# Optimization experiments

Measured on AMD Instinct MI355X. Metric: run time of the kernel, lower is better.

The kernel has to match this reference:

```python
import jax, jax.numpy as jnp
import numpy as np

N_NODES = 50000
N_EDGES = 800000
D_FEAT = 128


def setup_inputs() -> dict:
    key = jax.random.key(0)
    k1, k2, k3, k4, k5, k6 = jax.random.split(key, 6)
    input = jax.random.normal(k1, (N_NODES, D_FEAT), dtype=jnp.float32)
    h0 = jax.random.normal(k2, (N_NODES, D_FEAT), dtype=jnp.float32)
    # edge list + weights represent the sparse normalized adjacency used by torch.spmm
    edge_row = jax.random.randint(k3, (N_EDGES,), 0, N_NODES, dtype=jnp.int32)
    edge_col = jax.random.randint(k4, (N_EDGES,), 0, N_NODES, dtype=jnp.int32)
    edge_weight = jax.random.uniform(k5, (N_EDGES,), dtype=jnp.float32)
    # learned parameter: uniform(-stdv, stdv) with stdv = 1/sqrt(out_features)
    stdv = 1.0 / np.sqrt(D_FEAT)
    weight = jax.random.uniform(k6, (D_FEAT, D_FEAT), dtype=jnp.float32,
                                minval=-stdv, maxval=stdv)
    return {
        "input": input,
        "h0": h0,
        "weight": weight,
        "edge_row": edge_row,
        "edge_col": edge_col,
        "edge_weight": edge_weight,
        "lamda": jnp.float32(0.5),
        "alpha": jnp.float32(0.1),
        "l": 4,
    }


def reference(input, h0, weight, edge_row, edge_col, edge_weight, lamda, alpha, l):
    n = input.shape[0]
    # theta = min(1, log(lamda / l + 1))
    theta = jnp.minimum(jnp.float32(1.0), jnp.log(lamda / l + 1.0))
    # hi = spmm(adj, input): gather source features, scale by edge weight, scatter-add to dest rows
    hi = jax.ops.segment_sum(edge_weight[:, None] * input[edge_col], edge_row,
                             num_segments=n)  # [N, D]
    support = (1.0 - alpha) * hi + alpha * h0
    output = theta * (support @ weight) + (1.0 - theta) * support
    return output + input
```

## Files before the change

kernel.cpp:

```cpp
#include <hip/hip_runtime.h>
#include <hip/hip_fp16.h>

#define D_FEAT 128

typedef _Float16 half8_t __attribute__((ext_vector_type(8)));
typedef float float4_t __attribute__((ext_vector_type(4)));

__device__ __forceinline__ float h16_to_f(unsigned short u) {
    union { unsigned short u; _Float16 f; } cv; cv.u = u; return (float)cv.f;
}
__device__ __forceinline__ unsigned short f_to_h16(float f) {
    union { unsigned short u; _Float16 f; } cv; cv.f = (_Float16)f; return cv.u;
}

__global__ __launch_bounds__(256) void prep_kernel(
    const float* __restrict__ input, unsigned* __restrict__ inph_u2,
    const float* __restrict__ W, __half* __restrict__ wt16,
    unsigned* __restrict__ sedge4_slack,
    const int* __restrict__ erow, int* __restrict__ bucket_cnt,
    int nconv4, int n_edges, int convBlocks, int wBlocks)
{
    __shared__ int lh[256];
    const int bid = blockIdx.x;
    const int t = threadIdx.x;

    if (bid < convBlocks) {
        int tid = bid * 256 + t;
        if (tid < nconv4) {
            float4 v = reinterpret_cast<const float4*>(input)[tid];
            __half2 a = __floats2half2_rn(v.x, v.y);
            __half2 b = __floats2half2_rn(v.z, v.w);
            uint2 p;
            p.x = *reinterpret_cast<unsigned*>(&a);
            p.y = *reinterpret_cast<unsigned*>(&b);
            reinterpret_cast<uint2*>(inph_u2)[tid] = p;
        }
    } else if (bid < convBlocks + wBlocks) {
        int idx = (bid - convBlocks) * 256 + t;
        if (idx < D_FEAT * D_FEAT) {
            int n = idx >> 7, k = idx & 127;
            wt16[n * D_FEAT + k] = __float2half(W[k * D_FEAT + n]);
        }
    } else if (bid == convBlocks + wBlocks) {
        if (t < 16) sedge4_slack[t] = 0u;
    } else {
        int hb = bid - convBlocks - wBlocks - 1;
        lh[t] = 0;
        __syncthreads();
        int base = hb * 4096;
        int end = base + 4096; if (end > n_edges) end = n_edges;
        for (int i = base + t; i < end; i += 256)
            atomicAdd(&lh[erow[i] >> 8], 1);
        __syncthreads();
        int c = lh[t];
        if (c > 0) atomicAdd(&bucket_cnt[t], c);
    }
}

__global__ __launch_bounds__(256) void bucket_scan_kernel(
    const int* __restrict__ bucket_cnt, int* __restrict__ bcursor,
    int* __restrict__ bbase, int nb, int n_edges)
{
    __shared__ int lds[256];
    int t = threadIdx.x;
    int v = (t < nb) ? bucket_cnt[t] : 0;
    lds[t] = v;
    __syncthreads();
#pragma unroll
    for (int off = 1; off < 256; off <<= 1) {
        int add = (t >= off) ? lds[t - off] : 0;
        __syncthreads();
        lds[t] += add;
        __syncthreads();
    }
    if (t < nb) {
        int ex = lds[t] - v;
        bcursor[t] = ex;
        bbase[t] = ex;
    }
    if (t == 0) bbase[nb] = n_edges;
}

__global__ __launch_bounds__(256) void bin_kernel(
    const int* __restrict__ erow, const int* __restrict__ ecol,
    const float* __restrict__ ew, int* __restrict__ bcursor,
    uint2* __restrict__ btmp, int n_edges)
{
    __shared__ int lcnt[256];
    const int t = threadIdx.x;
    const int base = blockIdx.x * 4096;
    lcnt[t] = 0;
    __syncthreads();

    unsigned rc[16];
    float    wv[16];
#pragma unroll
    for (int i = 0; i < 16; ++i) {
        int idx = base + i * 256 + t;
        if (idx < n_edges) {
            int r = erow[idx];
            rc[i] = ((unsigned)r << 16) | (unsigned)ecol[idx];
            wv[i] = ew[idx];
            atomicAdd(&lcnt[r >> 8], 1);
        } else {
            rc[i] = 0xFFFFFFFFu;
        }
    }
    __syncthreads();
    int c = lcnt[t];
    int gbase = (c > 0) ? atomicAdd(&bcursor[t], c) : 0;
    lcnt[t] = gbase;
    __syncthreads();
#pragma unroll
    for (int i = 0; i < 16; ++i) {
        if (rc[i] != 0xFFFFFFFFu) {
            int b = rc[i] >> 24;
            int pos = atomicAdd(&lcnt[b], 1);
            uint2 p;
            p.x = rc[i];
            p.y = __float_as_uint(wv[i]);
            btmp[pos] = p;
        }
    }
}

__global__ __launch_bounds__(256) void sort_kernel(
    const uint2* __restrict__ btmp, const int* __restrict__ bbase,
    int* __restrict__ cnt, int* __restrict__ beg,
    unsigned* __restrict__ sedge4, int n)
{
    __shared__ int lscan[256];
    __shared__ int lofs[256];
    const int b = blockIdx.x;
    const int t = threadIdx.x;
    const int lo = bbase[b];
    const int hi = bbase[b + 1];

    lscan[t] = 0;
    __syncthreads();
    for (int i = lo + t; i < hi; i += 256) {
        int rl = (btmp[i].x >> 16) & 255;
        atomicAdd(&lscan[rl], 1);
    }
    __syncthreads();
    int v = lscan[t];
    __syncthreads();
#pragma unroll
    for (int off = 1; off < 256; off <<= 1) {
        int add = (t >= off) ? lscan[t - off] : 0;
        __syncthreads();
        lscan[t] += add;
        __syncthreads();
    }
    int ex = lscan[t] - v;
    lofs[t] = ex;
    int row = b * 256 + t;
    if (row < n) {
        cnt[row] = v;
        beg[row] = lo + ex;
    }
    __syncthreads();
    for (int i = lo + t; i < hi; i += 256) {
        uint2 p = btmp[i];
        int rl = (p.x >> 16) & 255;
        int pos = atomicAdd(&lofs[rl], 1);
        float w = __uint_as_float(p.y);
        sedge4[lo + pos] = (p.x & 0xFFFFu) | ((unsigned)f_to_h16(w) << 16);
    }
}

__global__ __launch_bounds__(256) void spmm4_kernel(
    const __half2* __restrict__ inph, const float* __restrict__ h0,
    const int* __restrict__ begp, const int* __restrict__ cnt,
    const unsigned* __restrict__ sedge4,
    const float* __restrict__ alpha_p, __half2* __restrict__ s16out, int n)
{
    int lane = threadIdx.x & 63;
    int row  = blockIdx.x * 4 + (threadIdx.x >> 6);
    if (row >= n) return;

    int deg = cnt[row];
    int beg = begp[row];

    float2 a0 = {0.f, 0.f}, a1 = {0.f, 0.f}, a2 = {0.f, 0.f}, a3 = {0.f, 0.f};
    for (int e = 0; e < deg; e += 8) {
        unsigned r0 = sedge4[beg + e + 0];
        unsigned r1 = sedge4[beg + e + 1];
        unsigned r2 = sedge4[beg + e + 2];
        unsigned r3 = sedge4[beg + e + 3];
        unsigned r4 = sedge4[beg + e + 4];
        unsigned r5 = sedge4[beg + e + 5];
        unsigned r6 = sedge4[beg + e + 6];
        unsigned r7 = sedge4[beg + e + 7];
        __half2 v0 = inph[(size_t)(r0 & 0xFFFFu) * 64 + lane];
        __half2 v1 = inph[(size_t)(r1 & 0xFFFFu) * 64 + lane];
        __half2 v2 = inph[(size_t)(r2 & 0xFFFFu) * 64 + lane];
        __half2 v3 = inph[(size_t)(r3 & 0xFFFFu) * 64 + lane];
        __half2 v4 = inph[(size_t)(r4 & 0xFFFFu) * 64 + lane];
        __half2 v5 = inph[(size_t)(r5 & 0xFFFFu) * 64 + lane];
        __half2 v6 = inph[(size_t)(r6 & 0xFFFFu) * 64 + lane];
        __half2 v7 = inph[(size_t)(r7 & 0xFFFFu) * 64 + lane];
        float w0 = h16_to_f((e + 0 < deg) ? (unsigned short)(r0 >> 16) : (unsigned short)0);
        float w1 = h16_to_f((e + 1 < deg) ? (unsigned short)(r1 >> 16) : (unsigned short)0);
        float w2 = h16_to_f((e + 2 < deg) ? (unsigned short)(r2 >> 16) : (unsigned short)0);
        float w3 = h16_to_f((e + 3 < deg) ? (unsigned short)(r3 >> 16) : (unsigned short)0);
        float w4 = h16_to_f((e + 4 < deg) ? (unsigned short)(r4 >> 16) : (unsigned short)0);
        float w5 = h16_to_f((e + 5 < deg) ? (unsigned short)(r5 >> 16) : (unsigned short)0);
        float w6 = h16_to_f((e + 6 < deg) ? (unsigned short)(r6 >> 16) : (unsigned short)0);
        float w7 = h16_to_f((e + 7 < deg) ? (unsigned short)(r7 >> 16) : (unsigned short)0);
        float2 f;
        f = __half22float2(v0); a0.x = fmaf(w0, f.x, a0.x); a0.y = fmaf(w0, f.y, a0.y);
        f = __half22float2(v1); a1.x = fmaf(w1, f.x, a1.x); a1.y = fmaf(w1, f.y, a1.y);
        f = __half22float2(v2); a2.x = fmaf(w2, f.x, a2.x); a2.y = fmaf(w2, f.y, a2.y);
        f = __half22float2(v3); a3.x = fmaf(w3, f.x, a3.x); a3.y = fmaf(w3, f.y, a3.y);
        f = __half22float2(v4); a0.x = fmaf(w4, f.x, a0.x); a0.y = fmaf(w4, f.y, a0.y);
        f = __half22float2(v5); a1.x = fmaf(w5, f.x, a1.x); a1.y = fmaf(w5, f.y, a1.y);
        f = __half22float2(v6); a2.x = fmaf(w6, f.x, a2.x); a2.y = fmaf(w6, f.y, a2.y);
        f = __half22float2(v7); a3.x = fmaf(w7, f.x, a3.x); a3.y = fmaf(w7, f.y, a3.y);
    }
    float2 acc;
    acc.x = (a0.x + a1.x) + (a2.x + a3.x);
    acc.y = (a0.y + a1.y) + (a2.y + a3.y);

    const float alpha = alpha_p[0];
    const float oma   = 1.0f - alpha;
    float2 h = reinterpret_cast<const float2*>(h0)[(size_t)row * 64 + lane];
    float sx = fmaf(oma, acc.x, alpha * h.x);
    float sy = fmaf(oma, acc.y, alpha * h.y);
    s16out[(size_t)row * 64 + lane] = __floats2half2_rn(sx, sy);
}

__global__ __launch_bounds__(256) void gemm_mfma_kernel(
    const __half* __restrict__ s16, const __half* __restrict__ wt16,
    const float* __restrict__ input, float* __restrict__ out,
    const float* __restrict__ lamda_p, const int* __restrict__ l_p,
    int n_rows)
{
    const int wave = threadIdx.x >> 6;
    const int lane = threadIdx.x & 63;
    const int row0 = (blockIdx.x * 4 + wave) * 16;
    if (row0 >= n_rows) return;

    const int mr = lane & 15;
    const int kg = lane >> 4;

    const _Float16* sp = reinterpret_cast<const _Float16*>(s16);
    const _Float16* wp = reinterpret_cast<const _Float16*>(wt16);

    float4_t acc[8];
#pragma unroll
    for (int nt = 0; nt < 8; ++nt) acc[nt] = (float4_t){0.f, 0.f, 0.f, 0.f};

#pragma unroll
    for (int ks = 0; ks < 4; ++ks) {
        const int kofs = ks * 32 + kg * 8;
        half8_t a = *reinterpret_cast<const half8_t*>(
            sp + (size_t)(row0 + mr) * D_FEAT + kofs);
#pragma unroll
        for (int nt = 0; nt < 8; ++nt) {
            half8_t b = *reinterpret_cast<const half8_t*>(
                wp + (size_t)(nt * 16 + mr) * D_FEAT + kofs);
            acc[nt] = __builtin_amdgcn_mfma_f32_16x16x32_f16(a, b, acc[nt], 0, 0, 0);
        }
    }

    const float lamda = lamda_p[0];
    const float theta = fminf(1.0f, logf(lamda / (float)l_p[0] + 1.0f));
    const float om_theta = 1.0f - theta;

#pragma unroll
    for (int nt = 0; nt < 8; ++nt) {
#pragma unroll
        for (int r = 0; r < 4; ++r) {
            const int row = row0 + kg * 4 + r;
            const int col = nt * 16 + mr;
            const size_t idx = (size_t)row * D_FEAT + col;
            const float s = (float)sp[idx];
            out[idx] = fmaf(theta, acc[nt][r], fmaf(om_theta, s, input[idx]));
        }
    }
}

__global__ __launch_bounds__(256) void hist_kernel(
    const int* __restrict__ erow, int* __restrict__ cnt, int n_edges)
{
    int e = blockIdx.x * 256 + threadIdx.x;
    if (e < n_edges) atomicAdd(&cnt[erow[e]], 1);
}

__global__ __launch_bounds__(256) void prep_noW_kernel(
    const float* __restrict__ input, unsigned* __restrict__ inph_u2,
    const int* __restrict__ erow, int* __restrict__ cnt,
    int nconv4, int n_edges)
{
    int tid = blockIdx.x * 256 + threadIdx.x;
    if (tid < nconv4) {
        float4 v = reinterpret_cast<const float4*>(input)[tid];
        __half2 a = __floats2half2_rn(v.x, v.y);
        __half2 b = __floats2half2_rn(v.z, v.w);
        uint2 p;
        p.x = *reinterpret_cast<unsigned*>(&a);
        p.y = *reinterpret_cast<unsigned*>(&b);
        reinterpret_cast<uint2*>(inph_u2)[tid] = p;
    } else {
        int e = tid - nconv4;
        if (e < n_edges) atomicAdd(&cnt[erow[e]], 1);
    }
}

__global__ __launch_bounds__(256) void partial_kernel(
    const int* __restrict__ cnt, int* __restrict__ partial, int n)
{
    __shared__ int lds[4];
    int i = blockIdx.x * 256 + threadIdx.x;
    int v = (i < n) ? cnt[i] : 0;
#pragma unroll
    for (int off = 32; off > 0; off >>= 1) v += __shfl_down(v, off, 64);
    if ((threadIdx.x & 63) == 0) lds[threadIdx.x >> 6] = v;
    __syncthreads();
    if (threadIdx.x == 0)
        partial[blockIdx.x] = lds[0] + lds[1] + lds[2] + lds[3];
}

__global__ __launch_bounds__(256) void scan_partial_kernel(
    int* __restrict__ partial, int nb)
{
    __shared__ int lds[256];
    int t = threadIdx.x;
    int v = (t < nb) ? partial[t] : 0;
    lds[t] = v;
    __syncthreads();
#pragma unroll
    for (int off = 1; off < 256; off <<= 1) {
        int add = (t >= off) ? lds[t - off] : 0;
        __syncthreads();
        lds[t] += add;
        __syncthreads();
    }
    if (t < nb) partial[t] = lds[t] - v;
}

__global__ __launch_bounds__(256) void scan_final_kernel(
    const int* __restrict__ cnt, const int* __restrict__ partial,
    int* __restrict__ cursor, int n)
{
    __shared__ int lds[256];
    int t = threadIdx.x;
    int i = blockIdx.x * 256 + t;
    int v = (i < n) ? cnt[i] : 0;
    lds[t] = v;
    __syncthreads();
#pragma unroll
    for (int off = 1; off < 256; off <<= 1) {
        int add = (t >= off) ? lds[t - off] : 0;
        __syncthreads();
        lds[t] += add;
        __syncthreads();
    }
    if (i < n) cursor[i] = lds[t] - v + partial[blockIdx.x];
}

__global__ __launch_bounds__(256) void edge_scatter_kernel(
    const int* __restrict__ erow, const int* __restrict__ ecol,
    const float* __restrict__ ew, int* __restrict__ cursor,
    uint2* __restrict__ sedge, int n_edges)
{
    int e = blockIdx.x * 256 + threadIdx.x;
    if (e >= n_edges) return;
    int r = erow[e];
    int pos = atomicAdd(&cursor[r], 1);
    uint2 p;
    p.x = (unsigned)ecol[e];
    p.y = __float_as_uint(ew[e]);
    sedge[pos] = p;
}

__global__ __launch_bounds__(256) void spmm_fp16_kernel(
    const __half2* __restrict__ inph, const float* __restrict__ h0,
    const int* __restrict__ cursor, const int* __restrict__ cnt,
    const uint2* __restrict__ sedge,
    const float* __restrict__ alpha_p, float* __restrict__ outp, int n)
{
    int lane = threadIdx.x & 63;
    int row  = blockIdx.x * 4 + (threadIdx.x >> 6);
    if (row >= n) return;
    int deg = cnt[row];
    int beg = cursor[row] - deg;
    float2 accA = make_float2(0.f, 0.f), accB = make_float2(0.f, 0.f);
    int e = 0;
    for (; e + 2 <= deg; e += 2) {
        uint2 e0 = sedge[beg + e], e1 = sedge[beg + e + 1];
        __half2 v0 = inph[(size_t)e0.x * 64 + lane];
        __half2 v1 = inph[(size_t)e1.x * 64 + lane];
        float w0 = __uint_as_float(e0.y), w1 = __uint_as_float(e1.y);
        float2 f0 = __half22float2(v0), f1 = __half22float2(v1);
        accA.x = fmaf(w0, f0.x, accA.x); accA.y = fmaf(w0, f0.y, accA.y);
        accB.x = fmaf(w1, f1.x, accB.x); accB.y = fmaf(w1, f1.y, accB.y);
    }
    if (e < deg) {
        uint2 e0 = sedge[beg + e];
        __half2 v0 = inph[(size_t)e0.x * 64 + lane];
        float w0 = __uint_as_float(e0.y);
        float2 f0 = __half22float2(v0);
        accA.x = fmaf(w0, f0.x, accA.x); accA.y = fmaf(w0, f0.y, accA.y);
    }
    float2 acc; acc.x = accA.x + accB.x; acc.y = accA.y + accB.y;
    const float alpha = alpha_p[0], oma = 1.0f - alpha;
    float2 h = reinterpret_cast<const float2*>(h0)[(size_t)row * 64 + lane];
    float2 s;
    s.x = fmaf(oma, acc.x, alpha * h.x);
    s.y = fmaf(oma, acc.y, alpha * h.y);
    reinterpret_cast<float2*>(outp)[(size_t)row * 64 + lane] = s;
}

__global__ __launch_bounds__(256) void spmm_fp32_kernel(
    const float* __restrict__ input, const float* __restrict__ h0,
    const int* __restrict__ cursor, const int* __restrict__ cnt,
    const uint2* __restrict__ sedge,
    const float* __restrict__ alpha_p, float* __restrict__ outp, int n)
{
    int lane = threadIdx.x & 63;
    int row  = blockIdx.x * 4 + (threadIdx.x >> 6);
    if (row >= n) return;
    int deg = cnt[row];
    int beg = cursor[row] - deg;
    const float2* in2 = reinterpret_cast<const float2*>(input);
    float2 acc = make_float2(0.f, 0.f);
    for (int e = 0; e < deg; ++e) {
        uint2 ed = sedge[beg + e];
        float w = __uint_as_float(ed.y);
        float2 v = in2[(size_t)ed.x * 64 + lane];
        acc.x = fmaf(w, v.x, acc.x);
        acc.y = fmaf(w, v.y, acc.y);
    }
    const float alpha = alpha_p[0], oma = 1.0f - alpha;
    float2 h = reinterpret_cast<const float2*>(h0)[(size_t)row * 64 + lane];
    float2 s;
    s.x = fmaf(oma, acc.x, alpha * h.x);
    s.y = fmaf(oma, acc.y, alpha * h.y);
    reinterpret_cast<float2*>(outp)[(size_t)row * 64 + lane] = s;
}

__global__ __launch_bounds__(256) void fused_kernel(
    float* __restrict__ io, const float* __restrict__ input,
    const float* __restrict__ W,
    const float* __restrict__ lamda_p, const int* __restrict__ l_p,
    int n_rows)
{
    __shared__ float s_lds[2][D_FEAT];
    const int j = threadIdx.x & 127;
    const int r = threadIdx.x >> 7;
    float wcol[D_FEAT];
#pragma unroll
    for (int k = 0; k < D_FEAT; ++k) wcol[k] = W[k * D_FEAT + j];
    const float lamda = lamda_p[0];
    const float theta = fminf(1.0f, logf(lamda / (float)l_p[0] + 1.0f));
    const float om_theta = 1.0f - theta;
    for (int row0 = blockIdx.x * 2; row0 < n_rows; row0 += gridDim.x * 2) {
        const int row = row0 + r;
        const bool active = row < n_rows;
        float sj = 0.0f;
        if (active) {
            sj = io[(size_t)row * D_FEAT + j];
            s_lds[r][j] = sj;
        }
        __syncthreads();
        if (active) {
            float dot = 0.0f;
            const float4* s4 = reinterpret_cast<const float4*>(s_lds[r]);
#pragma unroll
            for (int k4 = 0; k4 < D_FEAT / 4; ++k4) {
                const float4 sv = s4[k4];
                dot = fmaf(sv.x, wcol[4 * k4 + 0], dot);
                dot = fmaf(sv.y, wcol[4 * k4 + 1], dot);
                dot = fmaf(sv.z, wcol[4 * k4 + 2], dot);
                dot = fmaf(sv.w, wcol[4 * k4 + 3], dot);
            }
            const size_t base = (size_t)row * D_FEAT + j;
            io[base] = fmaf(theta, dot, om_theta * sj) + input[base];
        }
        __syncthreads();
    }
}

extern "C" void kernel_launch(void* const* d_in, const int* in_sizes, int n_in,
                              void* d_out, int out_size, void* d_ws, size_t ws_size,
                              hipStream_t stream)
{
    const float* input = (const float*)d_in[0];
    const float* h0    = (const float*)d_in[1];
    const float* W     = (const float*)d_in[2];
    const int*   erow  = (const int*)d_in[3];
    const int*   ecol  = (const int*)d_in[4];
    const float* ew    = (const float*)d_in[5];
    const float* lamda = (const float*)d_in[6];
    const float* alpha = (const float*)d_in[7];
    const int*   l_p   = (const int*)d_in[8];
    float* out = (float*)d_out;

    const int n_nodes = in_sizes[0] / D_FEAT;
    const int n_edges = in_sizes[3];
    const int nb = (n_nodes + 255) / 256;
    const int nconv4 = n_nodes * D_FEAT / 4;

    char* p = (char*)d_ws;
    auto align16 = [](char* q) {
        return (char*)(((uintptr_t)q + 15) & ~(uintptr_t)15);
    };
    int* cnt      = (int*)p;                    p += (size_t)n_nodes * 4;
    int* beg      = (int*)p;                    p += (size_t)n_nodes * 4;
    int* bucket_cnt = (int*)p;                  p += 256 * 4;
    int* bcursor  = (int*)p;                    p += 257 * 4;
    int* bbase    = (int*)p;                    p += 257 * 4;
    p = align16(p);
    unsigned* sedge4 = (unsigned*)p;            p += ((size_t)n_edges + 16) * 4;
    p = align16(p);
    unsigned* inph  = (unsigned*)p;             p += (size_t)n_nodes * D_FEAT * 2;
    p = align16(p);
    char* unionp = p;
    uint2*  btmp = (uint2*)unionp;
    __half* s16  = (__half*)unionp;
    size_t union_bytes = (size_t)n_nodes * D_FEAT * 2;
    if ((size_t)n_edges * 8 > union_bytes) union_bytes = (size_t)n_edges * 8;
    p += union_bytes;
    p = align16(p);
    __half* wt16 = (__half*)p;                  p += (size_t)D_FEAT * D_FEAT * 2;
    const size_t need_new = (size_t)(p - (char*)d_ws);

    const bool use_new = (ws_size >= need_new) && (n_nodes < 65536) && (nb <= 256);

    if (use_new) {
        const int convBlocks = (nconv4 + 255) / 256;
        const int wBlocks = (D_FEAT * D_FEAT + 255) / 256;
        const int histBlocks = (n_edges + 4095) / 4096;
        const int totalBlocks = convBlocks + wBlocks + 1 + histBlocks;

        hipMemsetAsync(bucket_cnt, 0, 256 * sizeof(int), stream);
        prep_kernel<<<totalBlocks, 256, 0, stream>>>(
            input, inph, W, wt16, sedge4 + n_edges, erow, bucket_cnt,
            nconv4, n_edges, convBlocks, wBlocks);
        bucket_scan_kernel<<<1, 256, 0, stream>>>(
            bucket_cnt, bcursor, bbase, nb, n_edges);
        bin_kernel<<<histBlocks, 256, 0, stream>>>(
            erow, ecol, ew, bcursor, btmp, n_edges);
        sort_kernel<<<nb, 256, 0, stream>>>(
            btmp, bbase, cnt, beg, sedge4, n_nodes);
        spmm4_kernel<<<(n_nodes + 3) / 4, 256, 0, stream>>>(
            (const __half2*)inph, h0, beg, cnt, sedge4, alpha,
            (__half2*)s16, n_nodes);
        const int ntiles = (n_nodes + 15) / 16;
        gemm_mfma_kernel<<<(ntiles + 3) / 4, 256, 0, stream>>>(
            s16, wt16, input, out, lamda, l_p, n_nodes);
        return;
    }

    int*   fcnt     = (int*)d_ws;
    int*   fcursor  = fcnt + n_nodes;
    int*   fpartial = fcursor + n_nodes;
    uint2* fsedge   = (uint2*)(fpartial + 256);
    unsigned* finph = (unsigned*)(fsedge + n_edges);

    const size_t need_base = (size_t)(2 * n_nodes + 256) * 4 + (size_t)n_edges * 8;
    const size_t need_fp16 = need_base + (size_t)n_nodes * D_FEAT * 2;
    const bool use_fp16 = ws_size >= need_fp16;

    hipMemsetAsync(fcnt, 0, (size_t)n_nodes * sizeof(int), stream);

    if (use_fp16) {
        int total = nconv4 + n_edges;
        prep_noW_kernel<<<(total + 255) / 256, 256, 0, stream>>>(
            input, finph, erow, fcnt, nconv4, n_edges);
    } else {
        hist_kernel<<<(n_edges + 255) / 256, 256, 0, stream>>>(erow, fcnt, n_edges);
    }
    partial_kernel<<<nb, 256, 0, stream>>>(fcnt, fpartial, n_nodes);
    scan_partial_kernel<<<1, 256, 0, stream>>>(fpartial, nb);
    scan_final_kernel<<<nb, 256, 0, stream>>>(fcnt, fpartial, fcursor, n_nodes);
    edge_scatter_kernel<<<(n_edges + 255) / 256, 256, 0, stream>>>(
        erow, ecol, ew, fcursor, fsedge, n_edges);
    if (use_fp16) {
        spmm_fp16_kernel<<<(n_nodes + 3) / 4, 256, 0, stream>>>(
            (const __half2*)finph, h0, fcursor, fcnt, fsedge, alpha, out, n_nodes);
    } else {
        spmm_fp32_kernel<<<(n_nodes + 3) / 4, 256, 0, stream>>>(
            input, h0, fcursor, fcnt, fsedge, alpha, out, n_nodes);
    }
    fused_kernel<<<2048, 256, 0, stream>>>(out, input, W, lamda, l_p, n_nodes);
}
```

Before: 118.1 us.

## Replace global bucket atomics with per-block partition scan; widen SpMM unroll

The histogram blocks now write per-block bucket counts to a partition array instead of atomically adding into global bucket counters. A single-block scan turns these into per-block, per-bucket write offsets, which removes the memset, the global atomics in the binning kernel, and its register-staged two-pass structure. The SpMM gather loop is also unrolled from 8 to 16 edges to keep more loads in flight. The single-block scan walks about 196 partition rows serially, which adds latency, and the wider unroll raises register pressure.

```diff
diff --git a/kernel.cpp b/kernel.cpp
--- a/kernel.cpp
+++ b/kernel.cpp
@@ -17,7 +17,7 @@
     const float* __restrict__ input, unsigned* __restrict__ inph_u2,
     const float* __restrict__ W, __half* __restrict__ wt16,
     unsigned* __restrict__ sedge4_slack,
-    const int* __restrict__ erow, int* __restrict__ bucket_cnt,
+    const int* __restrict__ erow, int* __restrict__ part,
     int nconv4, int n_edges, int convBlocks, int wBlocks)
 {
     __shared__ int lh[256];
@@ -52,19 +52,24 @@
         for (int i = base + t; i < end; i += 256)
             atomicAdd(&lh[erow[i] >> 8], 1);
         __syncthreads();
-        int c = lh[t];
-        if (c > 0) atomicAdd(&bucket_cnt[t], c);
-    }
-}
-
-__global__ __launch_bounds__(256) void bucket_scan_kernel(
-    const int* __restrict__ bucket_cnt, int* __restrict__ bcursor,
-    int* __restrict__ bbase, int nb, int n_edges)
+        part[hb * 256 + t] = lh[t];
+    }
+}
+
+__global__ __launch_bounds__(256) void pscan_kernel(
+    int* __restrict__ part, int* __restrict__ bbase,
+    int nb, int histBlocks, int n_edges)
 {
     __shared__ int lds[256];
-    int t = threadIdx.x;
-    int v = (t < nb) ? bucket_cnt[t] : 0;
-    lds[t] = v;
+    const int t = threadIdx.x;
+    int run = 0;
+    for (int hb = 0; hb < histBlocks; ++hb) {
+        int v = part[hb * 256 + t];
+        part[hb * 256 + t] = run;
+        run += v;
+    }
+    int tot = run;
+    lds[t] = tot;
     __syncthreads();
 #pragma unroll
     for (int off = 1; off < 256; off <<= 1) {
@@ -73,54 +78,32 @@
         lds[t] += add;
         __syncthreads();
     }
-    if (t < nb) {
-        int ex = lds[t] - v;
-        bcursor[t] = ex;
-        bbase[t] = ex;
-    }
-    if (t == 0) bbase[nb] = n_edges;
+    int ex = lds[t] - tot;
+    if (t <= nb) {
+        bbase[t] = (t < nb) ? ex : n_edges;
+    }
+    for (int hb = 0; hb < histBlocks; ++hb)
+        part[hb * 256 + t] += ex;
 }
 
 __global__ __launch_bounds__(256) void bin_kernel(
     const int* __restrict__ erow, const int* __restrict__ ecol,
-    const float* __restrict__ ew, int* __restrict__ bcursor,
+    const float* __restrict__ ew, const int* __restrict__ part,
     uint2* __restrict__ btmp, int n_edges)
 {
     __shared__ int lcnt[256];
     const int t = threadIdx.x;
     const int base = blockIdx.x * 4096;
-    lcnt[t] = 0;
-    __syncthreads();
-
-    unsigned rc[16];
-    float    wv[16];
-#pragma unroll
-    for (int i = 0; i < 16; ++i) {
-        int idx = base + i * 256 + t;
-        if (idx < n_edges) {
-            int r = erow[idx];
-            rc[i] = ((unsigned)r << 16) | (unsigned)ecol[idx];
-            wv[i] = ew[idx];
-            atomicAdd(&lcnt[r >> 8], 1);
-        } else {
-            rc[i] = 0xFFFFFFFFu;
-        }
-    }
-    __syncthreads();
-    int c = lcnt[t];
-    int gbase = (c > 0) ? atomicAdd(&bcursor[t], c) : 0;
-    lcnt[t] = gbase;
-    __syncthreads();
-#pragma unroll
-    for (int i = 0; i < 16; ++i) {
-        if (rc[i] != 0xFFFFFFFFu) {
-            int b = rc[i] >> 24;
-            int pos = atomicAdd(&lcnt[b], 1);
-            uint2 p;
-            p.x = rc[i];
-            p.y = __float_as_uint(wv[i]);
-            btmp[pos] = p;
-        }
+    lcnt[t] = part[blockIdx.x * 256 + t];
+    __syncthreads();
+    int end = base + 4096; if (end > n_edges) end = n_edges;
+    for (int i = base + t; i < end; i += 256) {
+        int r = erow[i];
+        int pos = atomicAdd(&lcnt[r >> 8], 1);
+        uint2 p;
+        p.x = ((unsigned)r << 16) | (unsigned)ecol[i];
+        p.y = __float_as_uint(ew[i]);
+        btmp[pos] = p;
     }
 }
 
@@ -183,40 +166,24 @@
     int beg = begp[row];
 
     float2 a0 = {0.f, 0.f}, a1 = {0.f, 0.f}, a2 = {0.f, 0.f}, a3 = {0.f, 0.f};
-    for (int e = 0; e < deg; e += 8) {
-        unsigned r0 = sedge4[beg + e + 0];
-        unsigned r1 = sedge4[beg + e + 1];
-        unsigned r2 = sedge4[beg + e + 2];
-        unsigned r3 = sedge4[beg + e + 3];
-        unsigned r4 = sedge4[beg + e + 4];
-        unsigned r5 = sedge4[beg + e + 5];
-        unsigned r6 = sedge4[beg + e + 6];
-        unsigned r7 = sedge4[beg + e + 7];
-        __half2 v0 = inph[(size_t)(r0 & 0xFFFFu) * 64 + lane];
-        __half2 v1 = inph[(size_t)(r1 & 0xFFFFu) * 64 + lane];
-        __half2 v2 = inph[(size_t)(r2 & 0xFFFFu) * 64 + lane];
-        __half2 v3 = inph[(size_t)(r3 & 0xFFFFu) * 64 + lane];
-        __half2 v4 = inph[(size_t)(r4 & 0xFFFFu) * 64 + lane];
-        __half2 v5 = inph[(size_t)(r5 & 0xFFFFu) * 64 + lane];
-        __half2 v6 = inph[(size_t)(r6 & 0xFFFFu) * 64 + lane];
-        __half2 v7 = inph[(size_t)(r7 & 0xFFFFu) * 64 + lane];
-        float w0 = h16_to_f((e + 0 < deg) ? (unsigned short)(r0 >> 16) : (unsigned short)0);
-        float w1 = h16_to_f((e + 1 < deg) ? (unsigned short)(r1 >> 16) : (unsigned short)0);
-        float w2 = h16_to_f((e + 2 < deg) ? (unsigned short)(r2 >> 16) : (unsigned short)0);
-        float w3 = h16_to_f((e + 3 < deg) ? (unsigned short)(r3 >> 16) : (unsigned short)0);
-        float w4 = h16_to_f((e + 4 < deg) ? (unsigned short)(r4 >> 16) : (unsigned short)0);
-        float w5 = h16_to_f((e + 5 < deg) ? (unsigned short)(r5 >> 16) : (unsigned short)0);
-        float w6 = h16_to_f((e + 6 < deg) ? (unsigned short)(r6 >> 16) : (unsigned short)0);
-        float w7 = h16_to_f((e + 7 < deg) ? (unsigned short)(r7 >> 16) : (unsigned short)0);
-        float2 f;
-        f = __half22float2(v0); a0.x = fmaf(w0, f.x, a0.x); a0.y = fmaf(w0, f.y, a0.y);
-        f = __half22float2(v1); a1.x = fmaf(w1, f.x, a1.x); a1.y = fmaf(w1, f.y, a1.y);
-        f = __half22float2(v2); a2.x = fmaf(w2, f.x, a2.x); a2.y = fmaf(w2, f.y, a2.y);
-        f = __half22float2(v3); a3.x = fmaf(w3, f.x, a3.x); a3.y = fmaf(w3, f.y, a3.y);
-        f = __half22float2(v4); a0.x = fmaf(w4, f.x, a0.x); a0.y = fmaf(w4, f.y, a0.y);
-        f = __half22float2(v5); a1.x = fmaf(w5, f.x, a1.x); a1.y = fmaf(w5, f.y, a1.y);
-        f = __half22float2(v6); a2.x = fmaf(w6, f.x, a2.x); a2.y = fmaf(w6, f.y, a2.y);
-        f = __half22float2(v7); a3.x = fmaf(w7, f.x, a3.x); a3.y = fmaf(w7, f.y, a3.y);
+    for (int e = 0; e < deg; e += 16) {
+        unsigned r[16];
+#pragma unroll
+        for (int i = 0; i < 16; ++i) r[i] = sedge4[beg + e + i];
+        __half2 v[16];
+#pragma unroll
+        for (int i = 0; i < 16; ++i)
+            v[i] = inph[(size_t)(r[i] & 0xFFFFu) * 64 + lane];
+#pragma unroll
+        for (int i = 0; i < 16; ++i) {
+            float w = h16_to_f((e + i < deg) ? (unsigned short)(r[i] >> 16)
+                                             : (unsigned short)0);
+            float2 f = __half22float2(v[i]);
+            if ((i & 3) == 0) { a0.x = fmaf(w, f.x, a0.x); a0.y = fmaf(w, f.y, a0.y); }
+            if ((i & 3) == 1) { a1.x = fmaf(w, f.x, a1.x); a1.y = fmaf(w, f.y, a1.y); }
+            if ((i & 3) == 2) { a2.x = fmaf(w, f.x, a2.x); a2.y = fmaf(w, f.y, a2.y); }
+            if ((i & 3) == 3) { a3.x = fmaf(w, f.x, a3.x); a3.y = fmaf(w, f.y, a3.y); }
+        }
     }
     float2 acc;
     acc.x = (a0.x + a1.x) + (a2.x + a3.x);
@@ -502,6 +469,7 @@
     const int n_edges = in_sizes[3];
     const int nb = (n_nodes + 255) / 256;
     const int nconv4 = n_nodes * D_FEAT / 4;
+    const int histBlocks = (n_edges + 4095) / 4096;
 
     char* p = (char*)d_ws;
     auto align16 = [](char* q) {
@@ -509,9 +477,8 @@
     };
     int* cnt      = (int*)p;                    p += (size_t)n_nodes * 4;
     int* beg      = (int*)p;                    p += (size_t)n_nodes * 4;
-    int* bucket_cnt = (int*)p;                  p += 256 * 4;
-    int* bcursor  = (int*)p;                    p += 257 * 4;
     int* bbase    = (int*)p;                    p += 257 * 4;
+    int* part     = (int*)p;                    p += (size_t)histBlocks * 256 * 4;
     p = align16(p);
     unsigned* sedge4 = (unsigned*)p;            p += ((size_t)n_edges + 16) * 4;
     p = align16(p);
@@ -532,17 +499,15 @@
     if (use_new) {
         const int convBlocks = (nconv4 + 255) / 256;
         const int wBlocks = (D_FEAT * D_FEAT + 255) / 256;
-        const int histBlocks = (n_edges + 4095) / 4096;
         const int totalBlocks = convBlocks + wBlocks + 1 + histBlocks;
 
-        hipMemsetAsync(bucket_cnt, 0, 256 * sizeof(int), stream);
         prep_kernel<<<totalBlocks, 256, 0, stream>>>(
-            input, inph, W, wt16, sedge4 + n_edges, erow, bucket_cnt,
+            input, inph, W, wt16, sedge4 + n_edges, erow, part,
             nconv4, n_edges, convBlocks, wBlocks);
-        bucket_scan_kernel<<<1, 256, 0, stream>>>(
-            bucket_cnt, bcursor, bbase, nb, n_edges);
+        pscan_kernel<<<1, 256, 0, stream>>>(
+            part, bbase, nb, histBlocks, n_edges);
         bin_kernel<<<histBlocks, 256, 0, stream>>>(
-            erow, ecol, ew, bcursor, btmp, n_edges);
+            erow, ecol, ew, part, btmp, n_edges);
         sort_kernel<<<nb, 256, 0, stream>>>(
             btmp, bbase, cnt, beg, sedge4, n_nodes);
         spmm4_kernel<<<(n_nodes + 3) / 4, 256, 0, stream>>>(
```

After: 168.8 us. 1.43x slower.

## Fuse SpMM with MFMA GEMM via LDS tile and fold bucket scan into prep

Applied to the files above, without the earlier changes.

The SpMM and GEMM kernels are merged. Each 256-thread block gathers 16 rows of support into an XOR-swizzled LDS tile, then runs MFMA against the fp16 weight, so the fp16 support intermediate never goes to global memory and is never read back. The separate single-block bucket-scan launch is removed: the last histogram block, found with an atomic ticket counter, performs the scan. This saves two kernel launches and an N×128 fp16 round trip, but each wave now walks 4 rows serially before a block barrier, which may cut latency hiding in the gather.

```diff
diff --git a/kernel.cpp b/kernel.cpp
--- a/kernel.cpp
+++ b/kernel.cpp
@@ -18,9 +18,13 @@
     const float* __restrict__ W, __half* __restrict__ wt16,
     unsigned* __restrict__ sedge4_slack,
     const int* __restrict__ erow, int* __restrict__ bucket_cnt,
-    int nconv4, int n_edges, int convBlocks, int wBlocks)
+    int* __restrict__ done_ctr, int* __restrict__ bcursor,
+    int* __restrict__ bbase,
+    int nconv4, int n_edges, int convBlocks, int wBlocks,
+    int histBlocks, int nb)
 {
     __shared__ int lh[256];
+    __shared__ int ticket_s;
     const int bid = blockIdx.x;
     const int t = threadIdx.x;
 
@@ -54,31 +58,29 @@
         __syncthreads();
         int c = lh[t];
         if (c > 0) atomicAdd(&bucket_cnt[t], c);
-    }
-}
-
-__global__ __launch_bounds__(256) void bucket_scan_kernel(
-    const int* __restrict__ bucket_cnt, int* __restrict__ bcursor,
-    int* __restrict__ bbase, int nb, int n_edges)
-{
-    __shared__ int lds[256];
-    int t = threadIdx.x;
-    int v = (t < nb) ? bucket_cnt[t] : 0;
-    lds[t] = v;
-    __syncthreads();
-#pragma unroll
-    for (int off = 1; off < 256; off <<= 1) {
-        int add = (t >= off) ? lds[t - off] : 0;
-        __syncthreads();
-        lds[t] += add;
-        __syncthreads();
-    }
-    if (t < nb) {
-        int ex = lds[t] - v;
-        bcursor[t] = ex;
-        bbase[t] = ex;
-    }
-    if (t == 0) bbase[nb] = n_edges;
+        __threadfence();
+        __syncthreads();
+        if (t == 0) ticket_s = atomicAdd(done_ctr, 1);
+        __syncthreads();
+        if (ticket_s == histBlocks - 1) {
+            int v = (t < nb) ? atomicAdd(&bucket_cnt[t], 0) : 0;
+            lh[t] = v;
+            __syncthreads();
+#pragma unroll
+            for (int off = 1; off < 256; off <<= 1) {
+                int add = (t >= off) ? lh[t - off] : 0;
+                __syncthreads();
+                lh[t] += add;
+                __syncthreads();
+            }
+            if (t < nb) {
+                int ex = lh[t] - v;
+                bcursor[t] = ex;
+                bbase[t] = ex;
+            }
+            if (t == 0) bbase[nb] = n_edges;
+        }
+    }
 }
 
 __global__ __launch_bounds__(256) void bin_kernel(
@@ -169,98 +171,97 @@
     }
 }
 
-__global__ __launch_bounds__(256) void spmm4_kernel(
+__global__ __launch_bounds__(256) void spmm_gemm_kernel(
     const __half2* __restrict__ inph, const float* __restrict__ h0,
     const int* __restrict__ begp, const int* __restrict__ cnt,
     const unsigned* __restrict__ sedge4,
-    const float* __restrict__ alpha_p, __half2* __restrict__ s16out, int n)
-{
-    int lane = threadIdx.x & 63;
-    int row  = blockIdx.x * 4 + (threadIdx.x >> 6);
-    if (row >= n) return;
-
-    int deg = cnt[row];
-    int beg = begp[row];
-
-    float2 a0 = {0.f, 0.f}, a1 = {0.f, 0.f}, a2 = {0.f, 0.f}, a3 = {0.f, 0.f};
-    for (int e = 0; e < deg; e += 8) {
-        unsigned r0 = sedge4[beg + e + 0];
-        unsigned r1 = sedge4[beg + e + 1];
-        unsigned r2 = sedge4[beg + e + 2];
-        unsigned r3 = sedge4[beg + e + 3];
-        unsigned r4 = sedge4[beg + e + 4];
-        unsigned r5 = sedge4[beg + e + 5];
-        unsigned r6 = sedge4[beg + e + 6];
-        unsigned r7 = sedge4[beg + e + 7];
-        __half2 v0 = inph[(size_t)(r0 & 0xFFFFu) * 64 + lane];
-        __half2 v1 = inph[(size_t)(r1 & 0xFFFFu) * 64 + lane];
-        __half2 v2 = inph[(size_t)(r2 & 0xFFFFu) * 64 + lane];
-        __half2 v3 = inph[(size_t)(r3 & 0xFFFFu) * 64 + lane];
-        __half2 v4 = inph[(size_t)(r4 & 0xFFFFu) * 64 + lane];
-        __half2 v5 = inph[(size_t)(r5 & 0xFFFFu) * 64 + lane];
-        __half2 v6 = inph[(size_t)(r6 & 0xFFFFu) * 64 + lane];
-        __half2 v7 = inph[(size_t)(r7 & 0xFFFFu) * 64 + lane];
-        float w0 = h16_to_f((e + 0 < deg) ? (unsigned short)(r0 >> 16) : (unsigned short)0);
-        float w1 = h16_to_f((e + 1 < deg) ? (unsigned short)(r1 >> 16) : (unsigned short)0);
-        float w2 = h16_to_f((e + 2 < deg) ? (unsigned short)(r2 >> 16) : (unsigned short)0);
-        float w3 = h16_to_f((e + 3 < deg) ? (unsigned short)(r3 >> 16) : (unsigned short)0);
-        float w4 = h16_to_f((e + 4 < deg) ? (unsigned short)(r4 >> 16) : (unsigned short)0);
-        float w5 = h16_to_f((e + 5 < deg) ? (unsigned short)(r5 >> 16) : (unsigned short)0);
-        float w6 = h16_to_f((e + 6 < deg) ? (unsigned short)(r6 >> 16) : (unsigned short)0);
-        float w7 = h16_to_f((e + 7 < deg) ? (unsigned short)(r7 >> 16) : (unsigned short)0);
-        float2 f;
-        f = __half22float2(v0); a0.x = fmaf(w0, f.x, a0.x); a0.y = fmaf(w0, f.y, a0.y);
-        f = __half22float2(v1); a1.x = fmaf(w1, f.x, a1.x); a1.y = fmaf(w1, f.y, a1.y);
-        f = __half22float2(v2); a2.x = fmaf(w2, f.x, a2.x); a2.y = fmaf(w2, f.y, a2.y);
-        f = __half22float2(v3); a3.x = fmaf(w3, f.x, a3.x); a3.y = fmaf(w3, f.y, a3.y);
-        f = __half22float2(v4); a0.x = fmaf(w4, f.x, a0.x); a0.y = fmaf(w4, f.y, a0.y);
-        f = __half22float2(v5); a1.x = fmaf(w5, f.x, a1.x); a1.y = fmaf(w5, f.y, a1.y);
-        f = __half22float2(v6); a2.x = fmaf(w6, f.x, a2.x); a2.y = fmaf(w6, f.y, a2.y);
-        f = __half22float2(v7); a3.x = fmaf(w7, f.x, a3.x); a3.y = fmaf(w7, f.y, a3.y);
-    }
-    float2 acc;
-    acc.x = (a0.x + a1.x) + (a2.x + a3.x);
-    acc.y = (a0.y + a1.y) + (a2.y + a3.y);
+    const float* __restrict__ alpha_p, const __half* __restrict__ wt16,
+    const float* __restrict__ input, float* __restrict__ out,
+    const float* __restrict__ lamda_p, const int* __restrict__ l_p,
+    int n)
+{
+    __shared__ _Float16 s_lds[16 * D_FEAT];
+    const int wave = threadIdx.x >> 6;
+    const int lane = threadIdx.x & 63;
+    const int row0 = blockIdx.x * 16;
 
     const float alpha = alpha_p[0];
     const float oma   = 1.0f - alpha;
-    float2 h = reinterpret_cast<const float2*>(h0)[(size_t)row * 64 + lane];
-    float sx = fmaf(oma, acc.x, alpha * h.x);
-    float sy = fmaf(oma, acc.y, alpha * h.y);
-    s16out[(size_t)row * 64 + lane] = __floats2half2_rn(sx, sy);
-}
-
-__global__ __launch_bounds__(256) void gemm_mfma_kernel(
-    const __half* __restrict__ s16, const __half* __restrict__ wt16,
-    const float* __restrict__ input, float* __restrict__ out,
-    const float* __restrict__ lamda_p, const int* __restrict__ l_p,
-    int n_rows)
-{
-    const int wave = threadIdx.x >> 6;
-    const int lane = threadIdx.x & 63;
-    const int row0 = (blockIdx.x * 4 + wave) * 16;
-    if (row0 >= n_rows) return;
+
+    for (int rr = 0; rr < 4; ++rr) {
+        const int r = wave * 4 + rr;
+        const int row = row0 + r;
+        float2 a0 = {0.f, 0.f}, a1 = {0.f, 0.f}, a2 = {0.f, 0.f}, a3 = {0.f, 0.f};
+        float sx = 0.0f, sy = 0.0f;
+        if (row < n) {
+            int deg = cnt[row];
+            int beg = begp[row];
+            for (int e = 0; e < deg; e += 8) {
+                unsigned r0 = sedge4[beg + e + 0];
+                unsigned r1 = sedge4[beg + e + 1];
+                unsigned r2 = sedge4[beg + e + 2];
+                unsigned r3 = sedge4[beg + e + 3];
+                unsigned r4 = sedge4[beg + e + 4];
+                unsigned r5 = sedge4[beg + e + 5];
+                unsigned r6 = sedge4[beg + e + 6];
+                unsigned r7 = sedge4[beg + e + 7];
+                __half2 v0 = inph[(size_t)(r0 & 0xFFFFu) * 64 + lane];
+                __half2 v1 = inph[(size_t)(r1 & 0xFFFFu) * 64 + lane];
+                __half2 v2 = inph[(size_t)(r2 & 0xFFFFu) * 64 + lane];
+                __half2 v3 = inph[(size_t)(r3 & 0xFFFFu) * 64 + lane];
+                __half2 v4 = inph[(size_t)(r4 & 0xFFFFu) * 64 + lane];
+                __half2 v5 = inph[(size_t)(r5 & 0xFFFFu) * 64 + lane];
+                __half2 v6 = inph[(size_t)(r6 & 0xFFFFu) * 64 + lane];
+                __half2 v7 = inph[(size_t)(r7 & 0xFFFFu) * 64 + lane];
+                float w0 = h16_to_f((e + 0 < deg) ? (unsigned short)(r0 >> 16) : (unsigned short)0);
+                float w1 = h16_to_f((e + 1 < deg) ? (unsigned short)(r1 >> 16) : (unsigned short)0);
+                float w2 = h16_to_f((e + 2 < deg) ? (unsigned short)(r2 >> 16) : (unsigned short)0);
+                float w3 = h16_to_f((e + 3 < deg) ? (unsigned short)(r3 >> 16) : (unsigned short)0);
+                float w4 = h16_to_f((e + 4 < deg) ? (unsigned short)(r4 >> 16) : (unsigned short)0);
+                float w5 = h16_to_f((e + 5 < deg) ? (unsigned short)(r5 >> 16) : (unsigned short)0);
+                float w6 = h16_to_f((e + 6 < deg) ? (unsigned short)(r6 >> 16) : (unsigned short)0);
+                float w7 = h16_to_f((e + 7 < deg) ? (unsigned short)(r7 >> 16) : (unsigned short)0);
+                float2 f;
+                f = __half22float2(v0); a0.x = fmaf(w0, f.x, a0.x); a0.y = fmaf(w0, f.y, a0.y);
+                f = __half22float2(v1); a1.x = fmaf(w1, f.x, a1.x); a1.y = fmaf(w1, f.y, a1.y);
+                f = __half22float2(v2); a2.x = fmaf(w2, f.x, a2.x); a2.y = fmaf(w2, f.y, a2.y);
+                f = __half22float2(v3); a3.x = fmaf(w3, f.x, a3.x); a3.y = fmaf(w3, f.y, a3.y);
+                f = __half22float2(v4); a0.x = fmaf(w4, f.x, a0.x); a0.y = fmaf(w4, f.y, a0.y);
+                f = __half22float2(v5); a1.x = fmaf(w5, f.x, a1.x); a1.y = fmaf(w5, f.y, a1.y);
+                f = __half22float2(v6); a2.x = fmaf(w6, f.x, a2.x); a2.y = fmaf(w6, f.y, a2.y);
+                f = __half22float2(v7); a3.x = fmaf(w7, f.x, a3.x); a3.y = fmaf(w7, f.y, a3.y);
+            }
+            float2 acc;
+            acc.x = (a0.x + a1.x) + (a2.x + a3.x);
+            acc.y = (a0.y + a1.y) + (a2.y + a3.y);
+            float2 h = reinterpret_cast<const float2*>(h0)[(size_t)row * 64 + lane];
+            sx = fmaf(oma, acc.x, alpha * h.x);
+            sy = fmaf(oma, acc.y, alpha * h.y);
+        }
+        const int byteW = r * 256 + ((lane * 4) ^ ((r & 7) << 4));
+        *reinterpret_cast<__half2*>(reinterpret_cast<char*>(s_lds) + byteW) =
+            __floats2half2_rn(sx, sy);
+    }
+    __syncthreads();
 
     const int mr = lane & 15;
     const int kg = lane >> 4;
 
-    const _Float16* sp = reinterpret_cast<const _Float16*>(s16);
-    const _Float16* wp = reinterpret_cast<const _Float16*>(wt16);
-
-    float4_t acc[8];
-#pragma unroll
-    for (int nt = 0; nt < 8; ++nt) acc[nt] = (float4_t){0.f, 0.f, 0.f, 0.f};
+    float4_t acc2[2];
+    acc2[0] = (float4_t){0.f, 0.f, 0.f, 0.f};
+    acc2[1] = (float4_t){0.f, 0.f, 0.f, 0.f};
 
 #pragma unroll
     for (int ks = 0; ks < 4; ++ks) {
-        const int kofs = ks * 32 + kg * 8;
+        const int byteA = mr * 256 + ((ks * 64 + kg * 16) ^ ((mr & 7) << 4));
         half8_t a = *reinterpret_cast<const half8_t*>(
-            sp + (size_t)(row0 + mr) * D_FEAT + kofs);
-#pragma unroll
-        for (int nt = 0; nt < 8; ++nt) {
+            reinterpret_cast<const char*>(s_lds) + byteA);
+#pragma unroll
+        for (int j = 0; j < 2; ++j) {
+            const int nt = wave * 2 + j;
             half8_t b = *reinterpret_cast<const half8_t*>(
-                wp + (size_t)(nt * 16 + mr) * D_FEAT + kofs);
-            acc[nt] = __builtin_amdgcn_mfma_f32_16x16x32_f16(a, b, acc[nt], 0, 0, 0);
+                wt16 + (size_t)(nt * 16 + mr) * D_FEAT + ks * 32 + kg * 8);
+            acc2[j] = __builtin_amdgcn_mfma_f32_16x16x32_f16(a, b, acc2[j], 0, 0, 0);
         }
     }
 
@@ -269,14 +270,19 @@
     const float om_theta = 1.0f - theta;
 
 #pragma unroll
-    for (int nt = 0; nt < 8; ++nt) {
-#pragma unroll
-        for (int r = 0; r < 4; ++r) {
-            const int row = row0 + kg * 4 + r;
-            const int col = nt * 16 + mr;
-            const size_t idx = (size_t)row * D_FEAT + col;
-            const float s = (float)sp[idx];
-            out[idx] = fmaf(theta, acc[nt][r], fmaf(om_theta, s, input[idx]));
+    for (int j = 0; j < 2; ++j) {
+        const int col = (wave * 2 + j) * 16 + mr;
+#pragma unroll
+        for (int rg = 0; rg < 4; ++rg) {
+            const int lr = kg * 4 + rg;
+            const int row = row0 + lr;
+            if (row < n) {
+                const int byteS = lr * 256 + ((2 * col) ^ ((lr & 7) << 4));
+                const float s = (float)*reinterpret_cast<const _Float16*>(
+                    reinterpret_cast<const char*>(s_lds) + byteS);
+                const size_t idx = (size_t)row * D_FEAT + col;
+                out[idx] = fmaf(theta, acc2[j][rg], fmaf(om_theta, s, input[idx]));
+            }
         }
     }
 }
@@ -502,27 +508,24 @@
     const int n_edges = in_sizes[3];
     const int nb = (n_nodes + 255) / 256;
     const int nconv4 = n_nodes * D_FEAT / 4;
+    const int histBlocks = (n_edges + 4095) / 4096;
 
     char* p = (char*)d_ws;
     auto align16 = [](char* q) {
         return (char*)(((uintptr_t)q + 15) & ~(uintptr_t)15);
     };
-    int* cnt      = (int*)p;                    p += (size_t)n_nodes * 4;
-    int* beg      = (int*)p;                    p += (size_t)n_nodes * 4;
+    int* cnt        = (int*)p;                  p += (size_t)n_nodes * 4;
+    int* beg        = (int*)p;                  p += (size_t)n_nodes * 4;
     int* bucket_cnt = (int*)p;                  p += 256 * 4;
-    int* bcursor  = (int*)p;                    p += 257 * 4;
-    int* bbase    = (int*)p;                    p += 257 * 4;
+    int* done_ctr   = (int*)p;                  p += 4;
+    int* bcursor    = (int*)p;                  p += 257 * 4;
+    int* bbase      = (int*)p;                  p += 257 * 4;
     p = align16(p);
     unsigned* sedge4 = (unsigned*)p;            p += ((size_t)n_edges + 16) * 4;
     p = align16(p);
     unsigned* inph  = (unsigned*)p;             p += (size_t)n_nodes * D_FEAT * 2;
     p = align16(p);
-    char* unionp = p;
-    uint2*  btmp = (uint2*)unionp;
-    __half* s16  = (__half*)unionp;
-    size_t union_bytes = (size_t)n_nodes * D_FEAT * 2;
-    if ((size_t)n_edges * 8 > union_bytes) union_bytes = (size_t)n_edges * 8;
-    p += union_bytes;
+    uint2* btmp = (uint2*)p;                    p += (size_t)n_edges * 8;
     p = align16(p);
     __half* wt16 = (__half*)p;                  p += (size_t)D_FEAT * D_FEAT * 2;
     const size_t need_new = (size_t)(p - (char*)d_ws);
@@ -532,25 +535,20 @@
     if (use_new) {
         const int convBlocks = (nconv4 + 255) / 256;
         const int wBlocks = (D_FEAT * D_FEAT + 255) / 256;
-        const int histBlocks = (n_edges + 4095) / 4096;
         const int totalBlocks = convBlocks + wBlocks + 1 + histBlocks;
 
-        hipMemsetAsync(bucket_cnt, 0, 256 * sizeof(int), stream);
+        hipMemsetAsync(bucket_cnt, 0, 257 * sizeof(int), stream);
         prep_kernel<<<totalBlocks, 256, 0, stream>>>(
             input, inph, W, wt16, sedge4 + n_edges, erow, bucket_cnt,
-            nconv4, n_edges, convBlocks, wBlocks);
-        bucket_scan_kernel<<<1, 256, 0, stream>>>(
-            bucket_cnt, bcursor, bbase, nb, n_edges);
+            done_ctr, bcursor, bbase,
+            nconv4, n_edges, convBlocks, wBlocks, histBlocks, nb);
         bin_kernel<<<histBlocks, 256, 0, stream>>>(
             erow, ecol, ew, bcursor, btmp, n_edges);
         sort_kernel<<<nb, 256, 0, stream>>>(
             btmp, bbase, cnt, beg, sedge4, n_nodes);
-        spmm4_kernel<<<(n_nodes + 3) / 4, 256, 0, stream>>>(
+        spmm_gemm_kernel<<<(n_nodes + 15) / 16, 256, 0, stream>>>(
             (const __half2*)inph, h0, beg, cnt, sedge4, alpha,
-            (__half2*)s16, n_nodes);
-        const int ntiles = (n_nodes + 15) / 16;
-        gemm_mfma_kernel<<<(ntiles + 3) / 4, 256, 0, stream>>>(
-            s16, wt16, input, out, lamda, l_p, n_nodes);
+            wt16, input, out, lamda, l_p, n_nodes);
         return;
     }
 
```

Result: slower. 124.6 us (+5.4%).
